# Kernel tuning notes

Hardware: AMD Instinct MI355X
Metric: run time of the kernel (lower is better)

The kernel has to match this reference:

```python
import jax, jax.numpy as jnp
import numpy as np

B, T, C = 2, 4096, 768
N_HEAD = 12
HEAD_DIM = C // N_HEAD


def setup_inputs() -> dict:
    key = jax.random.key(0)
    k1, k2, k3, k4, k5 = jax.random.split(key, 5)
    scale = 1.0 / np.sqrt(C)
    x = jax.random.normal(k1, (B, T, C), dtype=jnp.float32)
    # weights stored as [in, out] (transpose of torch Linear weight)
    W_attn = jax.random.normal(k2, (C, 3 * C), dtype=jnp.float32) * scale
    b_attn = jax.random.normal(k3, (3 * C,), dtype=jnp.float32) * 0.01
    W_proj = jax.random.normal(k4, (C, C), dtype=jnp.float32) * scale
    b_proj = jax.random.normal(k5, (C,), dtype=jnp.float32) * 0.01
    return {"x": x, "W_attn": W_attn, "b_attn": b_attn, "W_proj": W_proj, "b_proj": b_proj}


def reference(x, W_attn, b_attn, W_proj, b_proj):
    Bq, Tq, Cq = x.shape
    qkv = x @ W_attn + b_attn                      # [B, T, 3C]
    q, k, v = jnp.split(qkv, 3, axis=-1)           # each [B, T, C]

    def heads(t):
        return t.reshape(Bq, Tq, N_HEAD, HEAD_DIM).transpose(0, 2, 1, 3)  # [B, H, T, D]

    q, k, v = heads(q), heads(k), heads(v)
    att = jnp.einsum('bhqd,bhkd->bhqk', q, k) * (1.0 / np.sqrt(HEAD_DIM))  # [B, H, T, T]
    causal = jnp.tril(jnp.ones((Tq, Tq), dtype=bool))                      # [T, T]
    att = jnp.where(causal[None, None], att, jnp.finfo(att.dtype).min)
    att = jax.nn.softmax(att, axis=-1)
    y = jnp.einsum('bhqk,bhkd->bhqd', att, v)      # [B, H, T, D]
    y = y.transpose(0, 2, 1, 3).reshape(Bq, Tq, Cq)
    return y @ W_proj + b_proj
```

## Files before the change

### kernel.cpp

```cpp
#include <hip/hip_runtime.h>


#define TSEQ   4096
#define NHEAD  12
#define CDIM   768
#define C3     2304
#define BT_TOT 8192

typedef __bf16 bf16x8 __attribute__((ext_vector_type(8)));
typedef __bf16 bf16x2 __attribute__((ext_vector_type(2)));
typedef float  f32x4  __attribute__((ext_vector_type(4)));
typedef unsigned int u32x4 __attribute__((ext_vector_type(4)));

__device__ __forceinline__ unsigned short f2bf(float f) {
  unsigned int u = __builtin_bit_cast(unsigned int, f);
  u += 0x7FFFu + ((u >> 16) & 1u);
  return (unsigned short)(u >> 16);
}

__device__ __forceinline__ unsigned int pack2bf(float a, float b) {
  bf16x2 v = {(__bf16)a, (__bf16)b};
  return __builtin_bit_cast(unsigned int, v);
}

__device__ __forceinline__ f32x4 mfma16(bf16x8 a, bf16x8 b, f32x4 c) {
  return __builtin_amdgcn_mfma_f32_16x16x32_bf16(a, b, c, 0, 0, 0);
}

typedef const __attribute__((address_space(1))) void* gas_ptr;
typedef __attribute__((address_space(3))) void* las_ptr;


__global__ __launch_bounds__(256) void cast_f32_bf16(const float* __restrict__ x,
                                                     unsigned short* __restrict__ o, int n) {
  int i = (blockIdx.x * 256 + threadIdx.x) * 4;
  if (i < n) {
    float4 v = *(const float4*)(x + i);
    ushort4 u;
    u.x = f2bf(v.x); u.y = f2bf(v.y); u.z = f2bf(v.z); u.w = f2bf(v.w);
    *(ushort4*)(o + i) = u;
  }
}

__global__ __launch_bounds__(256) void transpose_cast(const float* __restrict__ src,
                                                      unsigned short* __restrict__ dst,
                                                      int K, int N) {
  __shared__ float tile[32][33];
  int n0 = blockIdx.x * 32, k0 = blockIdx.y * 32;
  int tx = threadIdx.x, ty = threadIdx.y;
#pragma unroll
  for (int i = 0; i < 4; ++i)
    tile[ty + i * 8][tx] = src[(size_t)(k0 + ty + i * 8) * N + n0 + tx];
  __syncthreads();
#pragma unroll
  for (int i = 0; i < 4; ++i)
    dst[(size_t)(n0 + ty + i * 8) * K + k0 + tx] = f2bf(tile[tx][ty + i * 8]);
}


__device__ __forceinline__ void stage_gemm(const unsigned short* __restrict__ A,
                                           const unsigned short* __restrict__ BTm,
                                           int K, int m0, int n0, int k0,
                                           unsigned short* buf, int wave,
                                           int srow, int scol) {
#pragma unroll
  for (int r = 0; r < 2; ++r) {
    const unsigned short* ga = A + (size_t)(m0 + r * 64 + srow) * K + k0 + scol;
    __builtin_amdgcn_global_load_lds((gas_ptr)ga,
        (las_ptr)(buf + r * 2048 + wave * 512), 16, 0, 0);
    const unsigned short* gb = BTm + (size_t)(n0 + r * 64 + srow) * K + k0 + scol;
    __builtin_amdgcn_global_load_lds((gas_ptr)gb,
        (las_ptr)(buf + 4096 + r * 2048 + wave * 512), 16, 0, 0);
  }
}

__device__ __forceinline__ void gemm_bt_mainloop(const unsigned short* __restrict__ A,
                                                 const unsigned short* __restrict__ BTm,
                                                 int K, int m0, int n0,
                                                 unsigned short* lds, f32x4 acc[4][4]) {
  const int tid = threadIdx.x;
  const int wave = tid >> 6, lane = tid & 63;
  const int quad = lane >> 4, l16 = lane & 15;
  const int wm = (wave >> 1) * 64, wn = (wave & 1) * 64;
  const int srow = tid >> 2;
  const int scol = (tid & 3) * 8;

  stage_gemm(A, BTm, K, m0, n0, 0, lds, wave, srow, scol);
  __syncthreads();

  int cur = 0;
  for (int k0 = 0; k0 < K; k0 += 32) {
    if (k0 + 32 < K)
      stage_gemm(A, BTm, K, m0, n0, k0 + 32, lds + (cur ^ 1) * 8192, wave, srow, scol);

    const unsigned short* buf = lds + cur * 8192;
    bf16x8 af[4], bfr[4];
#pragma unroll
    for (int i = 0; i < 4; ++i) {
      af[i]  = *(const bf16x8*)(buf + (wm + i * 16 + l16) * 32 + quad * 8);
      bfr[i] = *(const bf16x8*)(buf + 4096 + (wn + i * 16 + l16) * 32 + quad * 8);
    }
#pragma unroll
    for (int i = 0; i < 4; ++i)
#pragma unroll
      for (int j = 0; j < 4; ++j)
        acc[i][j] = mfma16(af[i], bfr[j], acc[i][j]);

    __syncthreads();
    cur ^= 1;
  }
}

__global__ __launch_bounds__(256, 4) void gemm_qkv_kernel(
    const unsigned short* __restrict__ A, const unsigned short* __restrict__ BTm,
    const float* __restrict__ bias,
    unsigned short* __restrict__ qbuf, unsigned short* __restrict__ kbuf,
    unsigned short* __restrict__ vtbuf) {
  __shared__ __align__(16) unsigned short lds[128 * 136];
  f32x4 zero = {0.f, 0.f, 0.f, 0.f};
  f32x4 acc[4][4];
#pragma unroll
  for (int i = 0; i < 4; ++i)
#pragma unroll
    for (int j = 0; j < 4; ++j) acc[i][j] = zero;

  const int m0 = blockIdx.y * 128, n0 = blockIdx.x * 128;
  gemm_bt_mainloop(A, BTm, CDIM, m0, n0, lds, acc);

  const int tid = threadIdx.x;
  const int wave = tid >> 6, lane = tid & 63;
  const int quad = lane >> 4, l16 = lane & 15;
  const int wm = (wave >> 1) * 64, wn = (wave & 1) * 64;
  const float KSCALE = 0.125f * 1.44269504088896340736f;

  const int seg = n0 / CDIM;
  const float mult = (seg == 1) ? KSCALE : 1.0f;

#pragma unroll
  for (int j = 0; j < 4; ++j) {
    const int nl = wn + j * 16 + l16;
    const float bv = bias[n0 + nl];
#pragma unroll
    for (int i = 0; i < 4; ++i) {
#pragma unroll
      for (int r = 0; r < 4; ++r) {
        const int ml = wm + i * 16 + quad * 4 + r;
        unsigned short val = f2bf((acc[i][j][r] + bv) * mult);
        if (seg < 2) lds[ml * 136 + nl] = val;
        else         lds[nl * 136 + ml] = val;
      }
    }
  }
  __syncthreads();

  const int row = tid >> 1, half = tid & 1;
  const unsigned short* src = lds + row * 136 + half * 64;
  if (seg < 2) {
    const int m = m0 + row, b = m >> 12, t = m & (TSEQ - 1);
    const int nn = (n0 - seg * CDIM) + half * 64;
    const int h = nn >> 6;
    unsigned short* base = (seg == 0) ? qbuf : kbuf;
    unsigned short* dst = base + ((size_t)(b * NHEAD + h) * TSEQ + t) * 64;
#pragma unroll
    for (int k = 0; k < 8; ++k)
      *(uint4*)(dst + k * 8) = *(const uint4*)(src + k * 8);
  } else {
    const int nn = (n0 - 2 * CDIM) + row;
    const int h = nn >> 6, d = nn & 63;
    const int b = m0 >> 12, t0 = (m0 & (TSEQ - 1)) + half * 64;
    unsigned short* dst = vtbuf + ((size_t)(b * NHEAD + h) * 64 + d) * TSEQ + t0;
#pragma unroll
    for (int k = 0; k < 8; ++k) {
      const int s0 = 32 * (k >> 2) + 4 * (k & 3);
      uint2 a = *(const uint2*)(src + s0);
      uint2 c = *(const uint2*)(src + s0 + 16);
      uint4 w = {a.x, a.y, c.x, c.y};
      *(uint4*)(dst + k * 8) = w;
    }
  }
}

__global__ __launch_bounds__(256, 4) void gemm_out_kernel(
    const unsigned short* __restrict__ A, const unsigned short* __restrict__ BTm,
    const float* __restrict__ bias, float* __restrict__ out) {
  __shared__ __align__(16) unsigned short lds[16384];
  f32x4 zero = {0.f, 0.f, 0.f, 0.f};
  f32x4 acc[4][4];
#pragma unroll
  for (int i = 0; i < 4; ++i)
#pragma unroll
    for (int j = 0; j < 4; ++j) acc[i][j] = zero;

  const int m0 = blockIdx.y * 128, n0 = blockIdx.x * 128;
  gemm_bt_mainloop(A, BTm, CDIM, m0, n0, lds, acc);

  const int tid = threadIdx.x;
  const int wave = tid >> 6, lane = tid & 63;
  const int quad = lane >> 4, l16 = lane & 15;
  const int wm = (wave >> 1) * 64, wn = (wave & 1) * 64;

#pragma unroll
  for (int j = 0; j < 4; ++j) {
    int n = n0 + wn + j * 16 + l16;
    float bv = bias[n];
#pragma unroll
    for (int i = 0; i < 4; ++i) {
#pragma unroll
      for (int r = 0; r < 4; ++r) {
        int m = m0 + wm + i * 16 + quad * 4 + r;
        out[(size_t)m * CDIM + n] = acc[i][j][r] + bv;
      }
    }
  }
}


__device__ __forceinline__ void stage_kv(const unsigned short* __restrict__ Kp,
                                         const unsigned short* __restrict__ Vp,
                                         int j0, unsigned short* kb, unsigned short* vb,
                                         int tid, int wave) {
  const int row = tid >> 3;
  const int col = ((tid & 7) ^ (row & 7)) * 8;
  __builtin_amdgcn_global_load_lds((gas_ptr)(Kp + (size_t)(j0 + row) * 64 + col),
                                   (las_ptr)(kb + wave * 512), 16, 0, 0);
  __builtin_amdgcn_global_load_lds((gas_ptr)(Vp + (size_t)row * TSEQ + j0 + col),
                                   (las_ptr)(vb + wave * 512), 16, 0, 0);
}

__device__ __forceinline__ void qk_score(const bf16x8 kf[8], const bf16x8 qf[2], f32x4 s[4]) {
  f32x4 zero = {0.f, 0.f, 0.f, 0.f};
#pragma unroll
  for (int i = 0; i < 4; ++i)
    s[i] = mfma16(kf[2 * i + 1], qf[1], mfma16(kf[2 * i], qf[0], zero));
}

template <bool MASKED>
__device__ __forceinline__ void exp_pack(const f32x4 s[4], int j0, int qabs,
                                         int l16, int quad, float& lsum, bf16x8 pf[2]) {
  unsigned int w[8];
#pragma unroll
  for (int i = 0; i < 4; ++i) {
    float p[4];
#pragma unroll
    for (int r = 0; r < 4; ++r) {
      p[r] = __builtin_amdgcn_exp2f(s[i][r]);
      if (MASKED) {
        if (j0 + i * 16 + quad * 4 + r > qabs) p[r] = 0.f;
      }
      lsum += p[r];
    }
    w[2 * i]     = pack2bf(p[0], p[1]);
    w[2 * i + 1] = pack2bf(p[2], p[3]);
  }
  u32x4 lo = {w[0], w[1], w[2], w[3]};
  u32x4 hi = {w[4], w[5], w[6], w[7]};
  pf[0] = __builtin_bit_cast(bf16x8, lo);
  pf[1] = __builtin_bit_cast(bf16x8, hi);
}

__device__ __forceinline__ void pv(const unsigned short* __restrict__ vb,
                                   int l16, int quad, int x7,
                                   const bf16x8 pf[2], f32x4 o[4]) {
#pragma unroll
  for (int dt = 0; dt < 4; ++dt) {
    const unsigned short* vr = vb + (dt * 16 + l16) * 64;
    bf16x8 v0 = *(const bf16x8*)(vr + ((quad ^ x7) * 8));
    bf16x8 v1 = *(const bf16x8*)(vr + (((4 + quad) ^ x7) * 8));
    o[dt] = mfma16(v1, pf[1], mfma16(v0, pf[0], o[dt]));
  }
}

__global__ __launch_bounds__(512, 6) void attn_kernel(const unsigned short* __restrict__ qbuf,
                                                      const unsigned short* __restrict__ kbuf,
                                                      const unsigned short* __restrict__ vtbuf,
                                                      unsigned short* __restrict__ y) {
  __shared__ __align__(16) unsigned short k_lds[2][64 * 64];
  __shared__ __align__(16) unsigned short v_lds[2][64 * 64];

  const int tid = threadIdx.x;
  const int wave = tid >> 6, lane = tid & 63;
  const int quad = lane >> 4, l16 = lane & 15;
  const int x7 = l16 & 7;

  const int bh = blockIdx.x % 24;
  const int p = blockIdx.x / 24;
  const bool isA = wave < 4;
  const int qtile = isA ? p : (63 - p);
  const int q0 = qtile * 64 + (wave & 3) * 16;

  const unsigned short* Qp = qbuf + (size_t)bh * TSEQ * 64;
  const unsigned short* Kp = kbuf + (size_t)bh * TSEQ * 64;
  const unsigned short* Vp = vtbuf + (size_t)bh * 64 * TSEQ;

  bf16x8 qf[2];
  qf[0] = *(const bf16x8*)(Qp + (size_t)(q0 + l16) * 64 + quad * 8);
  qf[1] = *(const bf16x8*)(Qp + (size_t)(q0 + l16) * 64 + 32 + quad * 8);

  f32x4 zero = {0.f, 0.f, 0.f, 0.f};
  f32x4 o[4];
#pragma unroll
  for (int dt = 0; dt < 4; ++dt) o[dt] = zero;
  float ls = 0.f;

  const int kcol0 = (quad ^ x7) * 8;
  const int ntiles = 64 - p;
  const int lasttile = isA ? p : (ntiles - 1);

  stage_kv(Kp, Vp, 0, k_lds[0], v_lds[0], tid, wave);

  for (int jt = 0; jt < ntiles; ++jt) {
    __syncthreads();
    if (jt + 1 < ntiles)
      stage_kv(Kp, Vp, (jt + 1) * 64, k_lds[(jt + 1) & 1], v_lds[(jt + 1) & 1], tid, wave);

    if (jt <= lasttile) {
      const unsigned short* kb = k_lds[jt & 1];
      const unsigned short* vb = v_lds[jt & 1];
      const int j0 = jt * 64;

      bf16x8 kf[8];
#pragma unroll
      for (int i = 0; i < 4; ++i) {
        kf[2 * i]     = *(const bf16x8*)(kb + (16 * i + l16) * 64 + kcol0);
        kf[2 * i + 1] = *(const bf16x8*)(kb + (16 * i + l16) * 64 + (kcol0 ^ 32));
      }

      f32x4 s[4];
      qk_score(kf, qf, s);

      bf16x8 pf[2];
      if (jt == lasttile) exp_pack<true>(s, j0, q0 + l16, l16, quad, ls, pf);
      else                exp_pack<false>(s, j0, q0 + l16, l16, quad, ls, pf);

      pv(vb, l16, quad, x7, pf, o);
    }
  }

  ls += __shfl_xor(ls, 16); ls += __shfl_xor(ls, 32);
  const float inv = 1.0f / ls;

  const int b = bh / NHEAD, hd = bh - b * NHEAD;
  unsigned short* yr = y + (size_t)(b * TSEQ + q0 + l16) * CDIM + hd * 64 + quad * 4;
#pragma unroll
  for (int dt = 0; dt < 4; ++dt) {
    uint2 w;
    w.x = pack2bf(o[dt][0] * inv, o[dt][1] * inv);
    w.y = pack2bf(o[dt][2] * inv, o[dt][3] * inv);
    *(uint2*)(yr + dt * 16) = w;
  }
}


extern "C" void kernel_launch(void* const* d_in, const int* in_sizes, int n_in,
                              void* d_out, int out_size, void* d_ws, size_t ws_size,
                              hipStream_t stream) {
  const float* x      = (const float*)d_in[0];
  const float* W_attn = (const float*)d_in[1];
  const float* b_attn = (const float*)d_in[2];
  const float* W_proj = (const float*)d_in[3];
  const float* b_proj = (const float*)d_in[4];
  float* out = (float*)d_out;

  unsigned short* xb    = (unsigned short*)d_ws;
  unsigned short* WaT   = xb + (size_t)BT_TOT * CDIM;
  unsigned short* WpT   = WaT + (size_t)C3 * CDIM;
  unsigned short* qbuf  = WpT + (size_t)CDIM * CDIM;
  unsigned short* kbuf  = qbuf + (size_t)2 * NHEAD * TSEQ * 64;
  unsigned short* vtbuf = kbuf + (size_t)2 * NHEAD * TSEQ * 64;
  unsigned short* ybuf  = xb;

  cast_f32_bf16<<<(BT_TOT * CDIM) / 1024, 256, 0, stream>>>(x, xb, BT_TOT * CDIM);
  transpose_cast<<<dim3(C3 / 32, CDIM / 32), dim3(32, 8), 0, stream>>>(W_attn, WaT, CDIM, C3);
  transpose_cast<<<dim3(CDIM / 32, CDIM / 32), dim3(32, 8), 0, stream>>>(W_proj, WpT, CDIM, CDIM);

  gemm_qkv_kernel<<<dim3(C3 / 128, BT_TOT / 128), 256, 0, stream>>>(xb, WaT, b_attn,
                                                                    qbuf, kbuf, vtbuf);
  attn_kernel<<<dim3(24 * 32), 512, 0, stream>>>(qbuf, kbuf, vtbuf, ybuf);
  gemm_out_kernel<<<dim3(CDIM / 128, BT_TOT / 128), 256, 0, stream>>>(ybuf, WpT, b_proj, out);
}
```

Before: 225.9 us.

## Process 32 query rows per wave in attention, halving block size to 256

Each attention wave now handles two 16-row query sub-tiles, so K fragments and V fragments read from LDS are reused across two MFMA chains. Blocks shrink from 8 to 4 waves, and each thread issues twice as many async global-to-LDS loads to stage the same 64x64 K/V tiles. This targets LDS read traffic per MFMA, at the cost of more registers per wave and fewer waves per block to hide latency.

```diff
diff --git a/kernel.cpp b/kernel.cpp
--- a/kernel.cpp
+++ b/kernel.cpp
@@ -215,16 +215,20 @@
 }
 
 
-__device__ __forceinline__ void stage_kv(const unsigned short* __restrict__ Kp,
-                                         const unsigned short* __restrict__ Vp,
-                                         int j0, unsigned short* kb, unsigned short* vb,
-                                         int tid, int wave) {
+__device__ __forceinline__ void stage_kv4(const unsigned short* __restrict__ Kp,
+                                          const unsigned short* __restrict__ Vp,
+                                          int j0, unsigned short* kb, unsigned short* vb,
+                                          int tid, int wave) {
   const int row = tid >> 3;
   const int col = ((tid & 7) ^ (row & 7)) * 8;
   __builtin_amdgcn_global_load_lds((gas_ptr)(Kp + (size_t)(j0 + row) * 64 + col),
                                    (las_ptr)(kb + wave * 512), 16, 0, 0);
+  __builtin_amdgcn_global_load_lds((gas_ptr)(Kp + (size_t)(j0 + 32 + row) * 64 + col),
+                                   (las_ptr)(kb + 2048 + wave * 512), 16, 0, 0);
   __builtin_amdgcn_global_load_lds((gas_ptr)(Vp + (size_t)row * TSEQ + j0 + col),
                                    (las_ptr)(vb + wave * 512), 16, 0, 0);
+  __builtin_amdgcn_global_load_lds((gas_ptr)(Vp + (size_t)(row + 32) * TSEQ + j0 + col),
+                                   (las_ptr)(vb + 2048 + wave * 512), 16, 0, 0);
 }
 
 __device__ __forceinline__ void qk_score(const bf16x8 kf[8], const bf16x8 qf[2], f32x4 s[4]) {
@@ -258,19 +262,21 @@
   pf[1] = __builtin_bit_cast(bf16x8, hi);
 }
 
-__device__ __forceinline__ void pv(const unsigned short* __restrict__ vb,
-                                   int l16, int quad, int x7,
-                                   const bf16x8 pf[2], f32x4 o[4]) {
+__device__ __forceinline__ void pv_dual(const unsigned short* __restrict__ vb,
+                                        int l16, int quad, int x7,
+                                        const bf16x8 pf0[2], const bf16x8 pf1[2],
+                                        f32x4 o0[4], f32x4 o1[4]) {
 #pragma unroll
   for (int dt = 0; dt < 4; ++dt) {
     const unsigned short* vr = vb + (dt * 16 + l16) * 64;
     bf16x8 v0 = *(const bf16x8*)(vr + ((quad ^ x7) * 8));
     bf16x8 v1 = *(const bf16x8*)(vr + (((4 + quad) ^ x7) * 8));
-    o[dt] = mfma16(v1, pf[1], mfma16(v0, pf[0], o[dt]));
-  }
-}
-
-__global__ __launch_bounds__(512, 6) void attn_kernel(const unsigned short* __restrict__ qbuf,
+    o0[dt] = mfma16(v1, pf0[1], mfma16(v0, pf0[0], o0[dt]));
+    o1[dt] = mfma16(v1, pf1[1], mfma16(v0, pf1[0], o1[dt]));
+  }
+}
+
+__global__ __launch_bounds__(256, 3) void attn_kernel(const unsigned short* __restrict__ qbuf,
                                                       const unsigned short* __restrict__ kbuf,
                                                       const unsigned short* __restrict__ vtbuf,
                                                       unsigned short* __restrict__ y) {
@@ -284,34 +290,36 @@
 
   const int bh = blockIdx.x % 24;
   const int p = blockIdx.x / 24;
-  const bool isA = wave < 4;
+  const bool isA = wave < 2;
   const int qtile = isA ? p : (63 - p);
-  const int q0 = qtile * 64 + (wave & 3) * 16;
+  const int q0 = qtile * 64 + (wave & 1) * 32;
 
   const unsigned short* Qp = qbuf + (size_t)bh * TSEQ * 64;
   const unsigned short* Kp = kbuf + (size_t)bh * TSEQ * 64;
   const unsigned short* Vp = vtbuf + (size_t)bh * 64 * TSEQ;
 
-  bf16x8 qf[2];
-  qf[0] = *(const bf16x8*)(Qp + (size_t)(q0 + l16) * 64 + quad * 8);
-  qf[1] = *(const bf16x8*)(Qp + (size_t)(q0 + l16) * 64 + 32 + quad * 8);
+  bf16x8 qf0[2], qf1[2];
+  qf0[0] = *(const bf16x8*)(Qp + (size_t)(q0 + l16) * 64 + quad * 8);
+  qf0[1] = *(const bf16x8*)(Qp + (size_t)(q0 + l16) * 64 + 32 + quad * 8);
+  qf1[0] = *(const bf16x8*)(Qp + (size_t)(q0 + 16 + l16) * 64 + quad * 8);
+  qf1[1] = *(const bf16x8*)(Qp + (size_t)(q0 + 16 + l16) * 64 + 32 + quad * 8);
 
   f32x4 zero = {0.f, 0.f, 0.f, 0.f};
-  f32x4 o[4];
-#pragma unroll
-  for (int dt = 0; dt < 4; ++dt) o[dt] = zero;
-  float ls = 0.f;
+  f32x4 o0[4], o1[4];
+#pragma unroll
+  for (int dt = 0; dt < 4; ++dt) { o0[dt] = zero; o1[dt] = zero; }
+  float ls0 = 0.f, ls1 = 0.f;
 
   const int kcol0 = (quad ^ x7) * 8;
   const int ntiles = 64 - p;
   const int lasttile = isA ? p : (ntiles - 1);
 
-  stage_kv(Kp, Vp, 0, k_lds[0], v_lds[0], tid, wave);
+  stage_kv4(Kp, Vp, 0, k_lds[0], v_lds[0], tid, wave);
 
   for (int jt = 0; jt < ntiles; ++jt) {
     __syncthreads();
     if (jt + 1 < ntiles)
-      stage_kv(Kp, Vp, (jt + 1) * 64, k_lds[(jt + 1) & 1], v_lds[(jt + 1) & 1], tid, wave);
+      stage_kv4(Kp, Vp, (jt + 1) * 64, k_lds[(jt + 1) & 1], v_lds[(jt + 1) & 1], tid, wave);
 
     if (jt <= lasttile) {
       const unsigned short* kb = k_lds[jt & 1];
@@ -325,28 +333,39 @@
         kf[2 * i + 1] = *(const bf16x8*)(kb + (16 * i + l16) * 64 + (kcol0 ^ 32));
       }
 
-      f32x4 s[4];
-      qk_score(kf, qf, s);
-
-      bf16x8 pf[2];
-      if (jt == lasttile) exp_pack<true>(s, j0, q0 + l16, l16, quad, ls, pf);
-      else                exp_pack<false>(s, j0, q0 + l16, l16, quad, ls, pf);
-
-      pv(vb, l16, quad, x7, pf, o);
-    }
-  }
-
-  ls += __shfl_xor(ls, 16); ls += __shfl_xor(ls, 32);
-  const float inv = 1.0f / ls;
+      f32x4 s0[4], s1[4];
+      qk_score(kf, qf0, s0);
+      qk_score(kf, qf1, s1);
+
+      bf16x8 pf0[2], pf1[2];
+      if (jt == lasttile) {
+        exp_pack<true>(s0, j0, q0 + l16,      l16, quad, ls0, pf0);
+        exp_pack<true>(s1, j0, q0 + 16 + l16, l16, quad, ls1, pf1);
+      } else {
+        exp_pack<false>(s0, j0, q0 + l16,      l16, quad, ls0, pf0);
+        exp_pack<false>(s1, j0, q0 + 16 + l16, l16, quad, ls1, pf1);
+      }
+
+      pv_dual(vb, l16, quad, x7, pf0, pf1, o0, o1);
+    }
+  }
+
+  ls0 += __shfl_xor(ls0, 16); ls0 += __shfl_xor(ls0, 32);
+  ls1 += __shfl_xor(ls1, 16); ls1 += __shfl_xor(ls1, 32);
+  const float inv0 = 1.0f / ls0, inv1 = 1.0f / ls1;
 
   const int b = bh / NHEAD, hd = bh - b * NHEAD;
-  unsigned short* yr = y + (size_t)(b * TSEQ + q0 + l16) * CDIM + hd * 64 + quad * 4;
+  unsigned short* yr0 = y + (size_t)(b * TSEQ + q0 + l16) * CDIM + hd * 64 + quad * 4;
+  unsigned short* yr1 = yr0 + (size_t)16 * CDIM;
 #pragma unroll
   for (int dt = 0; dt < 4; ++dt) {
-    uint2 w;
-    w.x = pack2bf(o[dt][0] * inv, o[dt][1] * inv);
-    w.y = pack2bf(o[dt][2] * inv, o[dt][3] * inv);
-    *(uint2*)(yr + dt * 16) = w;
+    uint2 w0, w1;
+    w0.x = pack2bf(o0[dt][0] * inv0, o0[dt][1] * inv0);
+    w0.y = pack2bf(o0[dt][2] * inv0, o0[dt][3] * inv0);
+    w1.x = pack2bf(o1[dt][0] * inv1, o1[dt][1] * inv1);
+    w1.y = pack2bf(o1[dt][2] * inv1, o1[dt][3] * inv1);
+    *(uint2*)(yr0 + dt * 16) = w0;
+    *(uint2*)(yr1 + dt * 16) = w1;
   }
 }
 
@@ -375,6 +394,6 @@
 
   gemm_qkv_kernel<<<dim3(C3 / 128, BT_TOT / 128), 256, 0, stream>>>(xb, WaT, b_attn,
                                                                     qbuf, kbuf, vtbuf);
-  attn_kernel<<<dim3(24 * 32), 512, 0, stream>>>(qbuf, kbuf, vtbuf, ybuf);
+  attn_kernel<<<dim3(24 * 32), 256, 0, stream>>>(qbuf, kbuf, vtbuf, ybuf);
   gemm_out_kernel<<<dim3(CDIM / 128, BT_TOT / 128), 256, 0, stream>>>(ybuf, WpT, b_proj, out);
 }
```

New measurement: 228.1 us. No clear change (+1.0%).
